# Kernel tuning notes

Hardware: AMD Instinct MI355X
Metric: run time of the kernel (lower is better)

Reference implementation:

```python
import jax, jax.numpy as jnp
import numpy as np

L, B, T, C, H, FF = 2, 2, 2048, 512, 8, 1024
HS = C // H  # head size
EPS = 1.1920929e-07  # torch float32 finfo eps (nn.RMSNorm default)


def setup_inputs() -> dict:
    key = jax.random.key(0)
    ks = jax.random.split(key, 20)
    s = 0.02
    return {
        "hidden": jax.random.normal(ks[0], (B, T, C), jnp.float32),
        "target": jax.random.normal(ks[1], (B, T, C), jnp.float32),
        # self-attn per-head projections (bias=False)
        "Wq_s": jax.random.normal(ks[2], (L, H, C, HS)) * s,
        "Wk_s": jax.random.normal(ks[3], (L, H, C, HS)) * s,
        "Wv_s": jax.random.normal(ks[4], (L, H, C, HS)) * s,
        "Wo_s": jax.random.normal(ks[5], (L, C, C)) * s,
        "bo_s": jnp.zeros((L, C)),
        # cross-attn per-head projections
        "Wq_x": jax.random.normal(ks[6], (L, H, C, HS)) * s,
        "Wk_x": jax.random.normal(ks[7], (L, H, C, HS)) * s,
        "Wv_x": jax.random.normal(ks[8], (L, H, C, HS)) * s,
        "Wo_x": jax.random.normal(ks[9], (L, C, C)) * s,
        "bo_x": jnp.zeros((L, C)),
        # FFN
        "W1": jax.random.normal(ks[10], (L, C, FF)) * s,
        "b1": jnp.zeros((L, FF)),
        "W2": jax.random.normal(ks[11], (L, FF, C)) * s,
        "b2": jnp.zeros((L, C)),
        # RMSNorm gains ln1..ln4
        "g1": jnp.ones((L, C)),
        "g2": jnp.ones((L, C)),
        "g3": jnp.ones((L, C)),
        "g4": jnp.ones((L, C)),
    }


def _rms(x, g):
    return x * jax.lax.rsqrt(jnp.mean(x * x, axis=-1, keepdims=True) + EPS) * g


def _attn(q_in, kv_in, Wq, Wk, Wv, Wo, bo, causal):
    # q_in: [B,Tq,C], kv_in: [B,Tk,C]; W*: [H,C,HS]
    q = jnp.einsum('btc,hcd->bhtd', q_in, Wq)
    k = jnp.einsum('bsc,hcd->bhsd', kv_in, Wk)
    v = jnp.einsum('bsc,hcd->bhsd', kv_in, Wv)
    wei = jnp.einsum('bhtd,bhsd->bhts', q, k) * (HS ** -0.5)  # [B,H,Tq,Tk]
    if causal:
        Tq, Tk = q_in.shape[1], kv_in.shape[1]
        mask = jnp.tril(jnp.ones((Tq, Tk), bool))
        wei = jnp.where(mask, wei, -jnp.inf)
    wei = jax.nn.softmax(wei, axis=-1)
    out = jnp.einsum('bhts,bhsd->bhtd', wei, v)
    out = out.transpose(0, 2, 1, 3).reshape(q_in.shape[0], q_in.shape[1], C)
    return out @ Wo + bo


def reference(hidden, target, Wq_s, Wk_s, Wv_s, Wo_s, bo_s,
              Wq_x, Wk_x, Wv_x, Wo_x, bo_x,
              W1, b1, W2, b2, g1, g2, g3, g4):
    t = target
    for l in range(L):
        # masked self-attention with RMSNorm pre-norm + residual
        t = t + _attn(_rms(t, g1[l]), _rms(t, g1[l]), Wq_s[l], Wk_s[l], Wv_s[l],
                      Wo_s[l], bo_s[l], causal=True)
        # cross-attention: K/V from ln2(hidden), Q from ln3(t)
        t = t + _attn(_rms(t, g3[l]), _rms(hidden, g2[l]), Wq_x[l], Wk_x[l], Wv_x[l],
                      Wo_x[l], bo_x[l], causal=False)
        # GELU FFN
        h = _rms(t, g4[l])
        t = t + (jax.nn.gelu(h @ W1[l] + b1[l], approximate=False) @ W2[l] + b2[l])
    return t
```

## Files before the change

kernel.cpp:

```cpp
#include <hip/hip_runtime.h>
#include <hip/hip_bf16.h>
#include <math.h>

#define L 2
#define B 2
#define T 2048
#define C 512
#define H 8
#define FF 1024
#define HS 64
#define EPSV 1.1920929e-07f

typedef __hip_bfloat16 bf16;
typedef __attribute__((ext_vector_type(8))) short short8;
typedef __attribute__((ext_vector_type(4))) float f32x4;

__device__ __forceinline__ float b2f(bf16 x) { return __bfloat162float(x); }

__device__ __forceinline__ void gl16(const unsigned short* g, unsigned short* l) {
    __builtin_amdgcn_global_load_lds(
        (const __attribute__((address_space(1))) unsigned int*)g,
        (__attribute__((address_space(3))) unsigned int*)l, 16, 0, 0);
}

__global__ void detect_k(const unsigned short* __restrict__ g1bits, int* __restrict__ flag) {
    if (threadIdx.x == 0 && blockIdx.x == 0)
        *flag = (g1bits[0] != (unsigned short)0x3F80u) ? 1 : 0;
}

__device__ __forceinline__ float ld_in(const void* p, size_t i, int fl) {
    return fl ? ((const float*)p)[i] : b2f(((const bf16*)p)[i]);
}

#define QKVT_TOT 1572864
#define WO_TOT 524288
#define W12_TOT 1048576
#define SM_TOT 9216
#define ACT_TOT 2097152

struct TrArgs {
    const void *Wq_s, *Wk_s, *Wv_s, *Wq_x, *Wk_x, *Wv_x, *Wo_s, *Wo_x, *W1, *W2;
    bf16 *cQKVs, *cQKVx, *cWoTs, *cWoTx, *cW1T, *cW2T;
    const int* flag;
};

__global__ __launch_bounds__(256) void prep_tr_k(TrArgs a) {
    __shared__ float tile[32][33];
    int bid = blockIdx.x;
    int fl = *a.flag;
    const void* src; bf16* dst;
    size_t sbase;
    int srcLD, dstLD, r0, c0;
    if (bid < 3072) {
        int pid = bid >> 5, t = bid & 31;
        int which = pid / 48, rem = pid % 48;
        int l = rem / 24, rem2 = rem % 24;
        int p = rem2 >> 3, hh = rem2 & 7;
        src = which ? (p == 0 ? a.Wq_x : p == 1 ? a.Wk_x : a.Wv_x)
                    : (p == 0 ? a.Wq_s : p == 1 ? a.Wk_s : a.Wv_s);
        dst = (which ? a.cQKVx : a.cQKVs) + (size_t)l * 786432 + (size_t)(p * 512 + hh * 64) * 512;
        sbase = (size_t)(l * 8 + hh) * 32768;
        srcLD = 64; dstLD = 512;
        r0 = (t >> 1) * 32; c0 = (t & 1) * 32;
    } else if (bid < 4096) {
        int b2 = bid - 3072, pid = b2 >> 8, t = b2 & 255;
        int which = pid >> 1, l = pid & 1;
        src = which ? a.Wo_x : a.Wo_s;
        dst = (which ? a.cWoTx : a.cWoTs) + (size_t)l * 262144;
        sbase = (size_t)l * 262144;
        srcLD = 512; dstLD = 512;
        r0 = (t >> 4) * 32; c0 = (t & 15) * 32;
    } else if (bid < 5120) {
        int b2 = bid - 4096, l = b2 >> 9, t = b2 & 511;
        src = a.W1; dst = a.cW1T + (size_t)l * 524288; sbase = (size_t)l * 524288;
        srcLD = 1024; dstLD = 512;
        r0 = (t >> 5) * 32; c0 = (t & 31) * 32;
    } else {
        int b2 = bid - 5120, l = b2 >> 9, t = b2 & 511;
        src = a.W2; dst = a.cW2T + (size_t)l * 524288; sbase = (size_t)l * 524288;
        srcLD = 512; dstLD = 1024;
        r0 = (t >> 4) * 32; c0 = (t & 15) * 32;
    }
    int tx = threadIdx.x & 31, ty = threadIdx.x >> 5;
#pragma unroll
    for (int i = 0; i < 4; i++)
        tile[ty + i * 8][tx] = ld_in(src, sbase + (size_t)(r0 + ty + i * 8) * srcLD + c0 + tx, fl);
    __syncthreads();
#pragma unroll
    for (int i = 0; i < 4; i++)
        dst[(size_t)(c0 + ty + i * 8) * dstLD + r0 + tx] = __float2bfloat16(tile[tx][ty + i * 8]);
}

#define ACTQ 1048576
struct SmArgs {
    const void* sm[8];
    const void *hidden, *target;
    bf16* smallDst;
    float *hid, *t_buf;
    const int* flag;
};

__global__ void prep_small_k(SmArgs s) {
    int i = blockIdx.x * 256 + threadIdx.x;
    int fl = *s.flag;
    if (i < SM_TOT) {
        const int cum[9] = {0, 1024, 2048, 4096, 5120, 6144, 7168, 8192, 9216};
        int k = 0;
        while (i >= cum[k + 1]) k++;
        s.smallDst[i] = __float2bfloat16(ld_in(s.sm[k], i - cum[k], fl));
        return;
    }
    int q = i - SM_TOT;
    if (q >= ACTQ) return;
    int half = q >= (ACTQ / 2);
    size_t e = (size_t)(q - half * (ACTQ / 2)) * 4;
    const void* src = half ? s.target : s.hidden;
    float* dstf = half ? s.t_buf : s.hid;
    if (fl) {
        *(float4*)(dstf + e) = *(const float4*)((const float*)src + e);
    } else {
        ushort4 u = *(const ushort4*)((const unsigned short*)src + e);
        float4 v;
        v.x = __uint_as_float((unsigned)u.x << 16);
        v.y = __uint_as_float((unsigned)u.y << 16);
        v.z = __uint_as_float((unsigned)u.z << 16);
        v.w = __uint_as_float((unsigned)u.w << 16);
        *(float4*)(dstf + e) = v;
    }
}

__global__ void write_out_k(const float* __restrict__ in, void* __restrict__ out, int n,
                            const int* __restrict__ flag) {
    int i = blockIdx.x * blockDim.x + threadIdx.x;
    if (i >= n) return;
    if (*flag) ((float*)out)[i] = in[i];
    else       ((bf16*)out)[i] = __float2bfloat16(in[i]);
}

__global__ void rmsnorm_k(const float* __restrict__ x, const bf16* __restrict__ g,
                          bf16* __restrict__ y) {
    int row = blockIdx.x;
    int tid = threadIdx.x;
    const float* xr = x + (size_t)row * C;
    float v0 = xr[tid], v1 = xr[tid + 256];
    __shared__ float red[256];
    red[tid] = v0 * v0 + v1 * v1;
    __syncthreads();
    for (int s = 128; s > 0; s >>= 1) {
        if (tid < s) red[tid] += red[tid + s];
        __syncthreads();
    }
    float sc = rsqrtf(red[0] / (float)C + EPSV);
    y[(size_t)row * C + tid] = __float2bfloat16(v0 * sc * b2f(g[tid]));
    y[(size_t)row * C + tid + 256] = __float2bfloat16(v1 * sc * b2f(g[tid + 256]));
}

__global__ void rmsnorm2_k(const float* __restrict__ xa, const bf16* __restrict__ ga,
                           bf16* __restrict__ ya, const float* __restrict__ xb,
                           const bf16* __restrict__ gb, bf16* __restrict__ yb) {
    int sel = blockIdx.y;
    const float* x = sel ? xb : xa;
    const bf16* g = sel ? gb : ga;
    bf16* y = sel ? yb : ya;
    int row = blockIdx.x;
    int tid = threadIdx.x;
    const float* xr = x + (size_t)row * C;
    float v0 = xr[tid], v1 = xr[tid + 256];
    __shared__ float red[256];
    red[tid] = v0 * v0 + v1 * v1;
    __syncthreads();
    for (int s = 128; s > 0; s >>= 1) {
        if (tid < s) red[tid] += red[tid + s];
        __syncthreads();
    }
    float sc = rsqrtf(red[0] / (float)C + EPSV);
    y[(size_t)row * C + tid] = __float2bfloat16(v0 * sc * b2f(g[tid]));
    y[(size_t)row * C + tid + 256] = __float2bfloat16(v1 * sc * b2f(g[tid + 256]));
}

struct GDesc {
    const bf16* A; const bf16* Bt; const bf16* bias; float* resid; bf16* out;
    int N, K, ldOut, ep, nblkx, blkofs;
};
struct GBatch { GDesc d[3]; int nd; };

__global__ __launch_bounds__(256) void gemm64_k(GBatch gb) {
    int bid = blockIdx.x;
    int di = 0;
    if (gb.nd > 1 && bid >= gb.d[1].blkofs) di = 1;
    if (gb.nd > 2 && bid >= gb.d[2].blkofs) di = 2;
    GDesc g = gb.d[di];
    int lb = bid - g.blkofs;
    int bx = lb % g.nblkx, by = lb / g.nblkx;
    int m0 = by * 64, n0 = bx * 64;

    __shared__ alignas(16) unsigned short As[2][64 * 64];
    __shared__ alignas(16) unsigned short Bs[2][64 * 64];
    int tid = threadIdx.x, lane = tid & 63, wave = tid >> 6;
    int wr = wave >> 1, wc = wave & 1, quad = lane >> 4, l15 = lane & 15;
    const unsigned short* Au = (const unsigned short*)g.A;
    const unsigned short* Bu = (const unsigned short*)g.Bt;

    int r0 = tid >> 3, sg = tid & 7;
    int gs = sg ^ (r0 & 7);
    const unsigned short* agp0 = Au + (size_t)(m0 + r0) * g.K + gs * 8;
    const unsigned short* agp1 = Au + (size_t)(m0 + r0 + 32) * g.K + gs * 8;
    const unsigned short* bgp0 = Bu + (size_t)(n0 + r0) * g.K + gs * 8;
    const unsigned short* bgp1 = Bu + (size_t)(n0 + r0 + 32) * g.K + gs * 8;
    int wofs = wave * 512;

    f32x4 zf = {0.f, 0.f, 0.f, 0.f};
    f32x4 acc[2][2];
    acc[0][0] = zf; acc[0][1] = zf; acc[1][0] = zf; acc[1][1] = zf;

    int sws0 = ((quad) ^ (l15 & 7)) * 8;
    int sws1 = ((4 + quad) ^ (l15 & 7)) * 8;
    int arow = wr * 32 + l15, brow = wc * 32 + l15;

    int nk = g.K >> 6;
    {
        gl16(agp0, &As[0][wofs]);
        gl16(agp1, &As[0][wofs + 2048]);
        gl16(bgp0, &Bs[0][wofs]);
        gl16(bgp1, &Bs[0][wofs + 2048]);
    }
    __syncthreads();
    int buf = 0;
    for (int kt = 0; kt < nk; kt++) {
        if (kt + 1 < nk) {
            int ko = (kt + 1) << 6;
            gl16(agp0 + ko, &As[buf ^ 1][wofs]);
            gl16(agp1 + ko, &As[buf ^ 1][wofs + 2048]);
            gl16(bgp0 + ko, &Bs[buf ^ 1][wofs]);
            gl16(bgp1 + ko, &Bs[buf ^ 1][wofs + 2048]);
        }
        const unsigned short* Ab = As[buf];
        const unsigned short* Bb = Bs[buf];
        short8 a0[2], b0[2], a1[2], b1[2];
#pragma unroll
        for (int i = 0; i < 2; i++) {
            int ra = (arow + i * 16) << 6, rb = (brow + i * 16) << 6;
            a0[i] = *(const short8*)(Ab + ra + sws0);
            a1[i] = *(const short8*)(Ab + ra + sws1);
            b0[i] = *(const short8*)(Bb + rb + sws0);
            b1[i] = *(const short8*)(Bb + rb + sws1);
        }
#pragma unroll
        for (int mi = 0; mi < 2; mi++)
#pragma unroll
            for (int ni = 0; ni < 2; ni++) {
                acc[mi][ni] =
                    __builtin_amdgcn_mfma_f32_16x16x32_bf16(a0[mi], b0[ni], acc[mi][ni], 0, 0, 0);
                acc[mi][ni] =
                    __builtin_amdgcn_mfma_f32_16x16x32_bf16(a1[mi], b1[ni], acc[mi][ni], 0, 0, 0);
            }
        __syncthreads();
        buf ^= 1;
    }

#pragma unroll
    for (int mi = 0; mi < 2; mi++) {
#pragma unroll
        for (int ni = 0; ni < 2; ni++) {
            int colg = n0 + wc * 32 + ni * 16 + l15;
            float bv = (g.ep == 1 || g.ep == 2) ? b2f(g.bias[colg]) : 0.f;
#pragma unroll
            for (int r2 = 0; r2 < 4; r2++) {
                int rowg = m0 + wr * 32 + mi * 16 + quad * 4 + r2;
                float v = acc[mi][ni][r2];
                if (g.ep == 0) {
                    g.out[(size_t)rowg * g.ldOut + colg] = __float2bfloat16(v);
                } else if (g.ep == 1) {
                    g.resid[(size_t)rowg * g.ldOut + colg] += v + bv;
                } else if (g.ep == 2) {
                    float u = v + bv;
                    g.out[(size_t)rowg * g.ldOut + colg] =
                        __float2bfloat16(0.5f * u * (1.f + erff(u * 0.70710678118654752f)));
                } else {
                    g.out[((size_t)((colg >> 11) * 512 + rowg) << 11) + (colg & 2047)] =
                        __float2bfloat16(v);
                }
            }
        }
    }
}

#define PST 72
__global__ __launch_bounds__(128) void attn_mfma_k(const bf16* __restrict__ qkv,
                                                   const bf16* __restrict__ vT,
                                                   bf16* __restrict__ attnout, int causal) {
    __shared__ alignas(16) unsigned short KsA[2][4096], VtA[2][4096];
    __shared__ unsigned short Ps[2][16 * PST];
    int qt = causal ? (gridDim.x - 1 - blockIdx.x) : blockIdx.x;
    int h = blockIdx.y, b = blockIdx.z;
    int tid = threadIdx.x, lane = tid & 63, w = tid >> 6;
    int quad = lane >> 4, l15 = lane & 15;
    const unsigned short* qk = (const unsigned short*)qkv;
    const unsigned short* vTp = (const unsigned short*)vT + ((size_t)b * 512 + h * 64) * T;
    size_t rowbase = (size_t)b * T;
    int koff = 512 + h * 64;
    unsigned short* Pw = Ps[w];
    bf16* Pwb = (bf16*)Pw;

    short8 aq0[2], aq1[2];
#pragma unroll
    for (int g = 0; g < 2; g++) {
        const unsigned short* qrow =
            qk + (rowbase + qt * 64 + w * 32 + g * 16 + l15) * 1536 + h * 64;
        aq0[g] = *(const short8*)(qrow + quad * 8);
        aq1[g] = *(const short8*)(qrow + 32 + quad * 8);
    }

    int srow = lane >> 3;
    int ssp = (lane & 7) ^ (srow & 7);

    f32x4 zf = {0.f, 0.f, 0.f, 0.f};
    f32x4 oacc[2][4];
#pragma unroll
    for (int g = 0; g < 2; g++)
#pragma unroll
        for (int i = 0; i < 4; i++) oacc[g][i] = zf;
    float lpart[2][4] = {{0.f, 0.f, 0.f, 0.f}, {0.f, 0.f, 0.f, 0.f}};

    int nT = causal ? (qt + 1) : (T / 64);

#pragma unroll
    for (int j = 0; j < 4; j++) {
        int c = w * 4 + j;
        int r = c * 8 + srow;
        gl16(qk + (rowbase + r) * 1536 + koff + ssp * 8, KsA[0] + c * 512);
        gl16(vTp + (size_t)r * T + ssp * 8, VtA[0] + c * 512);
    }
    __syncthreads();

    int buf = 0;
    for (int st = 0; st < nT; st++) {
        if (st + 1 < nT) {
#pragma unroll
            for (int j = 0; j < 4; j++) {
                int c = w * 4 + j;
                int r = c * 8 + srow;
                gl16(qk + (rowbase + (st + 1) * 64 + r) * 1536 + koff + ssp * 8,
                     KsA[buf ^ 1] + c * 512);
                gl16(vTp + (size_t)r * T + (st + 1) * 64 + ssp * 8, VtA[buf ^ 1] + c * 512);
            }
        }

        const unsigned short* Kb = KsA[buf];
        const unsigned short* Vb = VtA[buf];

        short8 bv0[4], bv1[4];
#pragma unroll
        for (int dj = 0; dj < 4; dj++) {
            int rr = dj * 16 + l15;
            bv0[dj] = *(const short8*)(Vb + rr * 64 + ((quad ^ (rr & 7)) * 8));
            bv1[dj] = *(const short8*)(Vb + rr * 64 + (((4 + quad) ^ (rr & 7)) * 8));
        }

        bool diag = causal && (st == qt);
#pragma unroll
        for (int g = 0; g < 2; g++) {
            f32x4 sacc[4];
#pragma unroll
            for (int i = 0; i < 4; i++) sacc[i] = zf;
#pragma unroll
            for (int ni = 0; ni < 4; ni++) {
                int rr = ni * 16 + l15;
                short8 bk0 = *(const short8*)(Kb + rr * 64 + ((quad ^ (rr & 7)) * 8));
                short8 bk1 = *(const short8*)(Kb + rr * 64 + (((4 + quad) ^ (rr & 7)) * 8));
                sacc[ni] = __builtin_amdgcn_mfma_f32_16x16x32_bf16(aq0[g], bk0, sacc[ni], 0, 0, 0);
                sacc[ni] = __builtin_amdgcn_mfma_f32_16x16x32_bf16(aq1[g], bk1, sacc[ni], 0, 0, 0);
            }

            int ql = w * 32 + g * 16 + quad * 4;
#pragma unroll
            for (int reg = 0; reg < 4; reg++) {
                float lp = 0.f;
#pragma unroll
                for (int ni = 0; ni < 4; ni++) {
                    int s_l = ni * 16 + l15;
                    float p = __expf(sacc[ni][reg] * 0.125f);
                    if (diag && s_l > ql + reg) p = 0.f;
                    lp += p;
                    Pwb[(quad * 4 + reg) * PST + s_l] = __float2bfloat16(p);
                }
                lpart[g][reg] += lp;
            }

            short8 ap0 = *(const short8*)(Pw + l15 * PST + quad * 8);
            short8 ap1 = *(const short8*)(Pw + l15 * PST + 32 + quad * 8);
#pragma unroll
            for (int dj = 0; dj < 4; dj++) {
                oacc[g][dj] = __builtin_amdgcn_mfma_f32_16x16x32_bf16(ap0, bv0[dj], oacc[g][dj], 0, 0, 0);
                oacc[g][dj] = __builtin_amdgcn_mfma_f32_16x16x32_bf16(ap1, bv1[dj], oacc[g][dj], 0, 0, 0);
            }
        }

        __syncthreads();
        buf ^= 1;
    }

#pragma unroll
    for (int g = 0; g < 2; g++)
#pragma unroll
        for (int reg = 0; reg < 4; reg++) {
#pragma unroll
            for (int mk = 1; mk < 16; mk <<= 1)
                lpart[g][reg] += __shfl_xor(lpart[g][reg], mk, 64);
            lpart[g][reg] = 1.0f / lpart[g][reg];
        }
#pragma unroll
    for (int g = 0; g < 2; g++)
#pragma unroll
        for (int dj = 0; dj < 4; dj++) {
            int d = dj * 16 + l15;
#pragma unroll
            for (int reg = 0; reg < 4; reg++) {
                int q = w * 32 + g * 16 + quad * 4 + reg;
                attnout[(rowbase + qt * 64 + q) * C + h * HS + d] =
                    __float2bfloat16(oacc[g][dj][reg] * lpart[g][reg]);
            }
        }
}

extern "C" void kernel_launch(void* const* d_in, const int* in_sizes, int n_in,
                              void* d_out, int out_size, void* d_ws, size_t ws_size,
                              hipStream_t stream) {
    const int BTC = B * T * C;
    const int BTF = B * T * FF;

    char* wsb = (char*)d_ws;
    int* flag = (int*)wsb;
    bf16* cur = (bf16*)(wsb + 256);
    bf16* cQKVs = cur;   cur += QKVT_TOT;
    bf16* cQKVx = cur;   cur += QKVT_TOT;
    bf16* cWoTs = cur;   cur += WO_TOT;
    bf16* cWoTx = cur;   cur += WO_TOT;
    bf16* cW1T = cur;    cur += W12_TOT;
    bf16* cW2T = cur;    cur += W12_TOT;
    bf16* smallBase = cur;
    bf16* cbo_s = cur;   cur += L * C;
    bf16* cbo_x = cur;   cur += L * C;
    bf16* cb1 = cur;     cur += L * FF;
    bf16* cb2 = cur;     cur += L * C;
    bf16* cg1 = cur;     cur += L * C;
    bf16* cg2 = cur;     cur += L * C;
    bf16* cg3 = cur;     cur += L * C;
    bf16* cg4 = cur;     cur += L * C;
    bf16* n1 = cur;      cur += BTC;
    bf16* n2 = cur;      cur += BTC;
    bf16* qkvbuf = cur;  cur += B * T * 3 * C;
    bf16* vTbuf = cur;   cur += BTC;
    bf16* attnout = cur; cur += BTC;
    bf16* h1buf = cur;   cur += BTF;
    size_t f32_off = (((char*)cur - wsb) + 255) & ~(size_t)255;
    float* t_buf = (float*)(wsb + f32_off);
    float* hid = t_buf + BTC;

    dim3 blk256(256);
    dim3 blk128(128);
    detect_k<<<1, 64, 0, stream>>>((const unsigned short*)d_in[16], flag);

    TrArgs ta;
    ta.Wq_s = d_in[2]; ta.Wk_s = d_in[3]; ta.Wv_s = d_in[4];
    ta.Wq_x = d_in[7]; ta.Wk_x = d_in[8]; ta.Wv_x = d_in[9];
    ta.Wo_s = d_in[5]; ta.Wo_x = d_in[10]; ta.W1 = d_in[12]; ta.W2 = d_in[14];
    ta.cQKVs = cQKVs; ta.cQKVx = cQKVx; ta.cWoTs = cWoTs; ta.cWoTx = cWoTx;
    ta.cW1T = cW1T; ta.cW2T = cW2T; ta.flag = flag;
    prep_tr_k<<<6144, blk256, 0, stream>>>(ta);

    SmArgs sa;
    sa.sm[0] = d_in[6];  sa.sm[1] = d_in[11]; sa.sm[2] = d_in[13]; sa.sm[3] = d_in[15];
    sa.sm[4] = d_in[16]; sa.sm[5] = d_in[17]; sa.sm[6] = d_in[18]; sa.sm[7] = d_in[19];
    sa.hidden = d_in[0]; sa.target = d_in[1];
    sa.smallDst = smallBase; sa.hid = hid; sa.t_buf = t_buf; sa.flag = flag;
    prep_small_k<<<(SM_TOT + ACTQ + 255) / 256, blk256, 0, stream>>>(sa);

    const int M = B * T;
    dim3 attngrid(T / 64, H, B);

    for (int l = 0; l < L; l++) {
        bf16* qkvW_s = cQKVs + (size_t)l * 3 * C * C;
        bf16* qkvW_x = cQKVx + (size_t)l * 3 * C * C;
        bf16* woT_s = cWoTs + (size_t)l * C * C;
        bf16* woT_x = cWoTx + (size_t)l * C * C;
        bf16* w1T = cW1T + (size_t)l * C * FF;
        bf16* w2T = cW2T + (size_t)l * FF * C;

        rmsnorm_k<<<M, blk256, 0, stream>>>(t_buf, cg1 + l * C, n1);
        {
            GBatch gb;
            gb.nd = 2;
            gb.d[0] = {n1, qkvW_s, nullptr, nullptr, qkvbuf, 1024, C, 3 * C, 0, 16, 0};
            gb.d[1] = {qkvW_s + (size_t)1024 * C, n1, nullptr, nullptr, vTbuf,
                       M, C, 0, 3, 64, 1024};
            gemm64_k<<<1024 + 512, blk256, 0, stream>>>(gb);
        }
        attn_mfma_k<<<attngrid, blk128, 0, stream>>>(qkvbuf, vTbuf, attnout, 1);
        {
            GBatch gb;
            gb.nd = 1;
            gb.d[0] = {attnout, woT_s, cbo_s + l * C, t_buf, nullptr, C, C, C, 1, 8, 0};
            gemm64_k<<<512, blk256, 0, stream>>>(gb);
        }

        rmsnorm2_k<<<dim3(M, 2), blk256, 0, stream>>>(t_buf, cg3 + l * C, n1, hid, cg2 + l * C, n2);
        {
            GBatch gb;
            gb.nd = 3;
            gb.d[0] = {n1, qkvW_x, nullptr, nullptr, qkvbuf, C, C, 3 * C, 0, 8, 0};
            gb.d[1] = {n2, qkvW_x + (size_t)512 * C, nullptr, nullptr, qkvbuf + C,
                       C, C, 3 * C, 0, 8, 512};
            gb.d[2] = {qkvW_x + (size_t)1024 * C, n2, nullptr, nullptr, vTbuf,
                       M, C, 0, 3, 64, 1024};
            gemm64_k<<<512 + 512 + 512, blk256, 0, stream>>>(gb);
        }
        attn_mfma_k<<<attngrid, blk128, 0, stream>>>(qkvbuf, vTbuf, attnout, 0);
        {
            GBatch gb;
            gb.nd = 1;
            gb.d[0] = {attnout, woT_x, cbo_x + l * C, t_buf, nullptr, C, C, C, 1, 8, 0};
            gemm64_k<<<512, blk256, 0, stream>>>(gb);
        }

        rmsnorm_k<<<M, blk256, 0, stream>>>(t_buf, cg4 + l * C, n1);
        {
            GBatch gb;
            gb.nd = 1;
            gb.d[0] = {n1, w1T, cb1 + l * FF, nullptr, h1buf, FF, C, FF, 2, 16, 0};
            gemm64_k<<<1024, blk256, 0, stream>>>(gb);
        }
        {
            GBatch gb;
            gb.nd = 1;
            gb.d[0] = {h1buf, w2T, cb2 + l * C, t_buf, nullptr, C, FF, C, 1, 8, 0};
            gemm64_k<<<512, blk256, 0, stream>>>(gb);
        }
    }

    write_out_k<<<(BTC + 255) / 256, blk256, 0, stream>>>(t_buf, d_out, BTC, flag);
}
```

Measured before the change: 585.4 us.

## Split attention KV range across four waves with per-wave buffers and LDS reduction

The attention kernel now uses 256 threads. Each of the four waves handles all 64 query rows of the tile but only every fourth 64-wide KV block, with its own K/V LDS buffers prefetched in place, so the per-iteration block-wide barrier goes away. Partial outputs and row sums are reduced across waves through shared memory at the end. This adds register pressure (16 accumulator tiles per wave), a larger LDS footprint (64KB plus), and load imbalance on short causal tiles where some waves have no work. Using unnormalized exp without a max subtraction is unchanged from before.

```diff
diff --git a/kernel.cpp b/kernel.cpp
--- a/kernel.cpp
+++ b/kernel.cpp
@@ -286,11 +286,11 @@
 }
 
 #define PST 72
-__global__ __launch_bounds__(128) void attn_mfma_k(const bf16* __restrict__ qkv,
+__global__ __launch_bounds__(256) void attn_mfma_k(const bf16* __restrict__ qkv,
                                                    const bf16* __restrict__ vT,
                                                    bf16* __restrict__ attnout, int causal) {
-    __shared__ alignas(16) unsigned short KsA[2][4096], VtA[2][4096];
-    __shared__ unsigned short Ps[2][16 * PST];
+    __shared__ alignas(16) unsigned short SMm[32768];
+    __shared__ alignas(16) unsigned short Ps[4][16 * PST];
     int qt = causal ? (gridDim.x - 1 - blockIdx.x) : blockIdx.x;
     int h = blockIdx.y, b = blockIdx.z;
     int tid = threadIdx.x, lane = tid & 63, w = tid >> 6;
@@ -299,14 +299,15 @@
     const unsigned short* vTp = (const unsigned short*)vT + ((size_t)b * 512 + h * 64) * T;
     size_t rowbase = (size_t)b * T;
     int koff = 512 + h * 64;
+    unsigned short* Kw = SMm + w * 4096;
+    unsigned short* Vw = SMm + 16384 + w * 4096;
     unsigned short* Pw = Ps[w];
     bf16* Pwb = (bf16*)Pw;
 
-    short8 aq0[2], aq1[2];
-#pragma unroll
-    for (int g = 0; g < 2; g++) {
-        const unsigned short* qrow =
-            qk + (rowbase + qt * 64 + w * 32 + g * 16 + l15) * 1536 + h * 64;
+    short8 aq0[4], aq1[4];
+#pragma unroll
+    for (int g = 0; g < 4; g++) {
+        const unsigned short* qrow = qk + (rowbase + qt * 64 + g * 16 + l15) * 1536 + h * 64;
         aq0[g] = *(const short8*)(qrow + quad * 8);
         aq1[g] = *(const short8*)(qrow + 32 + quad * 8);
     }
@@ -315,112 +316,146 @@
     int ssp = (lane & 7) ^ (srow & 7);
 
     f32x4 zf = {0.f, 0.f, 0.f, 0.f};
-    f32x4 oacc[2][4];
-#pragma unroll
-    for (int g = 0; g < 2; g++)
+    f32x4 oacc[4][4];
+#pragma unroll
+    for (int g = 0; g < 4; g++)
 #pragma unroll
         for (int i = 0; i < 4; i++) oacc[g][i] = zf;
-    float lpart[2][4] = {{0.f, 0.f, 0.f, 0.f}, {0.f, 0.f, 0.f, 0.f}};
+    float lpart[4][4];
+#pragma unroll
+    for (int g = 0; g < 4; g++)
+#pragma unroll
+        for (int r = 0; r < 4; r++) lpart[g][r] = 0.f;
 
     int nT = causal ? (qt + 1) : (T / 64);
 
-#pragma unroll
-    for (int j = 0; j < 4; j++) {
-        int c = w * 4 + j;
-        int r = c * 8 + srow;
-        gl16(qk + (rowbase + r) * 1536 + koff + ssp * 8, KsA[0] + c * 512);
-        gl16(vTp + (size_t)r * T + ssp * 8, VtA[0] + c * 512);
-    }
-    __syncthreads();
-
-    int buf = 0;
-    for (int st = 0; st < nT; st++) {
-        if (st + 1 < nT) {
-#pragma unroll
-            for (int j = 0; j < 4; j++) {
-                int c = w * 4 + j;
-                int r = c * 8 + srow;
-                gl16(qk + (rowbase + (st + 1) * 64 + r) * 1536 + koff + ssp * 8,
-                     KsA[buf ^ 1] + c * 512);
-                gl16(vTp + (size_t)r * T + (st + 1) * 64 + ssp * 8, VtA[buf ^ 1] + c * 512);
-            }
-        }
-
-        const unsigned short* Kb = KsA[buf];
-        const unsigned short* Vb = VtA[buf];
+    if (w < nT) {
+#pragma unroll
+        for (int c = 0; c < 8; c++) {
+            int r = c * 8 + srow;
+            gl16(qk + (rowbase + (size_t)w * 64 + r) * 1536 + koff + ssp * 8, Kw + c * 512);
+            gl16(vTp + (size_t)r * T + w * 64 + ssp * 8, Vw + c * 512);
+        }
+    }
+
+    for (int st = w; st < nT; st += 4) {
+        asm volatile("s_waitcnt vmcnt(0)" ::: "memory");
+        __builtin_amdgcn_sched_barrier(0);
+        int stn = st + 4;
+        bool diag = causal && (st == qt);
 
         short8 bv0[4], bv1[4];
 #pragma unroll
         for (int dj = 0; dj < 4; dj++) {
             int rr = dj * 16 + l15;
-            bv0[dj] = *(const short8*)(Vb + rr * 64 + ((quad ^ (rr & 7)) * 8));
-            bv1[dj] = *(const short8*)(Vb + rr * 64 + (((4 + quad) ^ (rr & 7)) * 8));
-        }
-
-        bool diag = causal && (st == qt);
-#pragma unroll
-        for (int g = 0; g < 2; g++) {
-            f32x4 sacc[4];
-#pragma unroll
-            for (int i = 0; i < 4; i++) sacc[i] = zf;
+            bv0[dj] = *(const short8*)(Vw + rr * 64 + ((quad ^ (rr & 7)) * 8));
+            bv1[dj] = *(const short8*)(Vw + rr * 64 + (((4 + quad) ^ (rr & 7)) * 8));
+        }
+        if (stn < nT) {
+            asm volatile("s_waitcnt lgkmcnt(0)" ::: "memory");
+            __builtin_amdgcn_sched_barrier(0);
+#pragma unroll
+            for (int c = 0; c < 8; c++) {
+                int r = c * 8 + srow;
+                gl16(vTp + (size_t)r * T + stn * 64 + ssp * 8, Vw + c * 512);
+            }
+        }
+
+#pragma unroll
+        for (int pass = 0; pass < 2; pass++) {
+            f32x4 sacc[2][4];
+#pragma unroll
+            for (int g2 = 0; g2 < 2; g2++)
+#pragma unroll
+                for (int i = 0; i < 4; i++) sacc[g2][i] = zf;
 #pragma unroll
             for (int ni = 0; ni < 4; ni++) {
                 int rr = ni * 16 + l15;
-                short8 bk0 = *(const short8*)(Kb + rr * 64 + ((quad ^ (rr & 7)) * 8));
-                short8 bk1 = *(const short8*)(Kb + rr * 64 + (((4 + quad) ^ (rr & 7)) * 8));
-                sacc[ni] = __builtin_amdgcn_mfma_f32_16x16x32_bf16(aq0[g], bk0, sacc[ni], 0, 0, 0);
-                sacc[ni] = __builtin_amdgcn_mfma_f32_16x16x32_bf16(aq1[g], bk1, sacc[ni], 0, 0, 0);
+                short8 bk0 = *(const short8*)(Kw + rr * 64 + ((quad ^ (rr & 7)) * 8));
+                short8 bk1 = *(const short8*)(Kw + rr * 64 + (((4 + quad) ^ (rr & 7)) * 8));
+#pragma unroll
+                for (int g2 = 0; g2 < 2; g2++) {
+                    int g = pass * 2 + g2;
+                    sacc[g2][ni] =
+                        __builtin_amdgcn_mfma_f32_16x16x32_bf16(aq0[g], bk0, sacc[g2][ni], 0, 0, 0);
+                    sacc[g2][ni] =
+                        __builtin_amdgcn_mfma_f32_16x16x32_bf16(aq1[g], bk1, sacc[g2][ni], 0, 0, 0);
+                }
             }
-
-            int ql = w * 32 + g * 16 + quad * 4;
-#pragma unroll
-            for (int reg = 0; reg < 4; reg++) {
-                float lp = 0.f;
-#pragma unroll
-                for (int ni = 0; ni < 4; ni++) {
-                    int s_l = ni * 16 + l15;
-                    float p = __expf(sacc[ni][reg] * 0.125f);
-                    if (diag && s_l > ql + reg) p = 0.f;
-                    lp += p;
-                    Pwb[(quad * 4 + reg) * PST + s_l] = __float2bfloat16(p);
+            if (pass == 1 && stn < nT) {
+                asm volatile("s_waitcnt lgkmcnt(0)" ::: "memory");
+                __builtin_amdgcn_sched_barrier(0);
+#pragma unroll
+                for (int c = 0; c < 8; c++) {
+                    int r = c * 8 + srow;
+                    gl16(qk + (rowbase + (size_t)stn * 64 + r) * 1536 + koff + ssp * 8,
+                         Kw + c * 512);
                 }
-                lpart[g][reg] += lp;
             }
-
-            short8 ap0 = *(const short8*)(Pw + l15 * PST + quad * 8);
-            short8 ap1 = *(const short8*)(Pw + l15 * PST + 32 + quad * 8);
-#pragma unroll
-            for (int dj = 0; dj < 4; dj++) {
-                oacc[g][dj] = __builtin_amdgcn_mfma_f32_16x16x32_bf16(ap0, bv0[dj], oacc[g][dj], 0, 0, 0);
-                oacc[g][dj] = __builtin_amdgcn_mfma_f32_16x16x32_bf16(ap1, bv1[dj], oacc[g][dj], 0, 0, 0);
+#pragma unroll
+            for (int g2 = 0; g2 < 2; g2++) {
+                int g = pass * 2 + g2;
+                int qrl = g * 16 + quad * 4;
+#pragma unroll
+                for (int reg = 0; reg < 4; reg++) {
+                    float lp = 0.f;
+#pragma unroll
+                    for (int ni = 0; ni < 4; ni++) {
+                        int s_l = ni * 16 + l15;
+                        float p = __expf(sacc[g2][ni][reg] * 0.125f);
+                        if (diag && s_l > qrl + reg) p = 0.f;
+                        lp += p;
+                        Pwb[(quad * 4 + reg) * PST + s_l] = __float2bfloat16(p);
+                    }
+                    lpart[g][reg] += lp;
+                }
+                short8 ap0 = *(const short8*)(Pw + l15 * PST + quad * 8);
+                short8 ap1 = *(const short8*)(Pw + l15 * PST + 32 + quad * 8);
+#pragma unroll
+                for (int dj = 0; dj < 4; dj++) {
+                    oacc[g][dj] =
+                        __builtin_amdgcn_mfma_f32_16x16x32_bf16(ap0, bv0[dj], oacc[g][dj], 0, 0, 0);
+                    oacc[g][dj] =
+                        __builtin_amdgcn_mfma_f32_16x16x32_bf16(ap1, bv1[dj], oacc[g][dj], 0, 0, 0);
+                }
             }
         }
-
-        __syncthreads();
-        buf ^= 1;
-    }
-
-#pragma unroll
-    for (int g = 0; g < 2; g++)
+    }
+
+#pragma unroll
+    for (int g = 0; g < 4; g++)
 #pragma unroll
         for (int reg = 0; reg < 4; reg++) {
 #pragma unroll
             for (int mk = 1; mk < 16; mk <<= 1)
                 lpart[g][reg] += __shfl_xor(lpart[g][reg], mk, 64);
-            lpart[g][reg] = 1.0f / lpart[g][reg];
-        }
-#pragma unroll
-    for (int g = 0; g < 2; g++)
-#pragma unroll
-        for (int dj = 0; dj < 4; dj++) {
-            int d = dj * 16 + l15;
-#pragma unroll
-            for (int reg = 0; reg < 4; reg++) {
-                int q = w * 32 + g * 16 + quad * 4 + reg;
-                attnout[(rowbase + qt * 64 + q) * C + h * HS + d] =
-                    __float2bfloat16(oacc[g][dj][reg] * lpart[g][reg]);
-            }
-        }
+        }
+
+    __syncthreads();
+    float* Ob = (float*)SMm;
+    float* Lb = (float*)Ps;
+#pragma unroll
+    for (int g = 0; g < 4; g++) {
+#pragma unroll
+        for (int dj = 0; dj < 4; dj++)
+#pragma unroll
+            for (int reg = 0; reg < 4; reg++)
+                Ob[w * 4096 + (g * 16 + quad * 4 + reg) * 64 + dj * 16 + l15] = oacc[g][dj][reg];
+        if (l15 == 0)
+#pragma unroll
+            for (int reg = 0; reg < 4; reg++)
+                Lb[w * 64 + g * 16 + quad * 4 + reg] = lpart[g][reg];
+    }
+    __syncthreads();
+
+#pragma unroll
+    for (int ql = 0; ql < 16; ql++) {
+        int q = w * 16 + ql;
+        float s = Ob[q * 64 + lane] + Ob[4096 + q * 64 + lane] +
+                  Ob[8192 + q * 64 + lane] + Ob[12288 + q * 64 + lane];
+        float lsum = Lb[q] + Lb[64 + q] + Lb[128 + q] + Lb[192 + q];
+        attnout[(rowbase + qt * 64 + q) * C + h * HS + lane] = __float2bfloat16(s / lsum);
+    }
 }
 
 extern "C" void kernel_launch(void* const* d_in, const int* in_sizes, int n_in,
@@ -458,7 +493,6 @@
     float* hid = t_buf + BTC;
 
     dim3 blk256(256);
-    dim3 blk128(128);
     detect_k<<<1, 64, 0, stream>>>((const unsigned short*)d_in[16], flag);
 
     TrArgs ta;
@@ -496,7 +530,7 @@
                        M, C, 0, 3, 64, 1024};
             gemm64_k<<<1024 + 512, blk256, 0, stream>>>(gb);
         }
-        attn_mfma_k<<<attngrid, blk128, 0, stream>>>(qkvbuf, vTbuf, attnout, 1);
+        attn_mfma_k<<<attngrid, blk256, 0, stream>>>(qkvbuf, vTbuf, attnout, 1);
         {
             GBatch gb;
             gb.nd = 1;
@@ -515,7 +549,7 @@
                        M, C, 0, 3, 64, 1024};
             gemm64_k<<<512 + 512 + 512, blk256, 0, stream>>>(gb);
         }
-        attn_mfma_k<<<attngrid, blk128, 0, stream>>>(qkvbuf, vTbuf, attnout, 0);
+        attn_mfma_k<<<attngrid, blk256, 0, stream>>>(qkvbuf, vTbuf, attnout, 0);
         {
             GBatch gb;
             gb.nd = 1;
```

After: 580.4 us. Within noise of the previous version (-0.8%).
